# Optimization experiments

Hardware: AMD Instinct MI355X
Metric: run time of the kernel (lower is better)

Reference implementation:

```python
import jax, jax.numpy as jnp
import numpy as np

N = 100000      # nodes
E = 1600000     # edges (avg degree 16)
IN = 128        # in_channels
C = 32          # out_channels per head
H = 4           # heads
NEG_SLOPE = 0.2 # PyG GATConv leaky_relu slope


def setup_inputs() -> dict:
    key = jax.random.key(0)
    k = jax.random.split(key, 6)
    x = jax.random.normal(k[0], (N, IN), jnp.float32)
    edge_index = jax.random.randint(k[1], (2, E), 0, N, jnp.int32)
    # glorot-ish init for learned params
    W = jax.random.normal(k[2], (IN, H * C), jnp.float32) * (2.0 / (IN + H * C)) ** 0.5
    att_src = jax.random.normal(k[3], (H, C), jnp.float32) * (1.0 / C) ** 0.5
    att_dst = jax.random.normal(k[4], (H, C), jnp.float32) * (1.0 / C) ** 0.5
    bias = jnp.zeros((C,), jnp.float32)
    return {"x": x, "edge_index": edge_index, "W": W,
            "att_src": att_src, "att_dst": att_dst, "bias": bias}


def reference(x, edge_index, W, att_src, att_dst, bias):
    n = x.shape[0]
    h_heads, c = att_src.shape
    # add self loops (PyG GATConv default add_self_loops=True)
    loop = jnp.arange(n, dtype=edge_index.dtype)
    src = jnp.concatenate([edge_index[0], loop])
    dst = jnp.concatenate([edge_index[1], loop])
    # shared linear projection for src and dst (single-tensor input in PyG)
    h = (x @ W).reshape(n, h_heads, c)                 # [N,H,C]
    a_src = jnp.sum(h * att_src, axis=-1)              # [N,H]
    a_dst = jnp.sum(h * att_dst, axis=-1)              # [N,H]
    # per-edge attention logits
    e = jax.nn.leaky_relu(a_src[src] + a_dst[dst], NEG_SLOPE)  # [E',H]
    # segment softmax over incoming edges of each dst node
    m = jax.ops.segment_max(e, dst, num_segments=n)    # [N,H]
    m = jax.lax.stop_gradient(jnp.where(jnp.isfinite(m), m, 0.0))
    p = jnp.exp(e - m[dst])
    denom = jax.ops.segment_sum(p, dst, num_segments=n)
    alpha = p / (denom[dst] + 1e-16)                   # [E',H]
    # weighted message scatter-add
    msg = h[src] * alpha[:, :, None]                   # [E',H,C]
    out = jax.ops.segment_sum(msg, dst, num_segments=n)  # [N,H,C]
    out = out.mean(axis=1) + bias                      # concat=False -> head mean
    return jax.nn.relu(out)                            # trailing act layer
```

## Files before the change

### kernel.cpp

```cpp
#include <hip/hip_runtime.h>

#define NODES 100000
#define NEDGE 1600000
#define ET (NEDGE + NODES)
#define INC 128
#define CC 32
#define HH 4
#define NEG 0.2f
#define CAP 48
#define PB 512
#define BB 1024
#define BSTRIDE (BB * 256)
#define NPASS 7

typedef __attribute__((ext_vector_type(8))) short short8;
typedef __attribute__((ext_vector_type(4))) float f32x4;
typedef __attribute__((ext_vector_type(8))) unsigned short u16x8;

static __device__ inline unsigned short f2bf(float f) {
    unsigned u = __float_as_uint(f);
    u += 0x7FFFu + ((u >> 16) & 1u);
    return (unsigned short)(u >> 16);
}
static __device__ inline float bf2f(unsigned short s) {
    return __uint_as_float((unsigned)s << 16);
}
static __device__ inline float lexp(float v) {
    v = v > 0.f ? v : NEG * v;
    return __expf(v);
}

__global__ __launch_bounds__(256) void k_mega(const float* __restrict__ x,
        const float* __restrict__ W, const float* __restrict__ att_src,
        const float* __restrict__ att_dst, const int* __restrict__ ei,
        unsigned short* __restrict__ hb, float* __restrict__ av,
        int* __restrict__ deg, int* __restrict__ bucket) {
    const int tid = threadIdx.x;

    if (blockIdx.x >= PB) {
        const int bid = blockIdx.x - PB;
        const int e0 = bid * 256 + tid;
        int sv[NPASS], dv[NPASS], slot[NPASS];
        #pragma unroll
        for (int p = 0; p < NPASS; ++p) {
            int e = e0 + p * BSTRIDE;
            sv[p] = -1;
            if (e < ET) {
                if (e < NEDGE) { sv[p] = ei[e]; dv[p] = ei[NEDGE + e]; }
                else           { sv[p] = e - NEDGE; dv[p] = e - NEDGE; }
            }
        }
        #pragma unroll
        for (int p = 0; p < NPASS; ++p)
            if (sv[p] >= 0) slot[p] = atomicAdd(&deg[dv[p]], 1);
        #pragma unroll
        for (int p = 0; p < NPASS; ++p)
            if (sv[p] >= 0) bucket[dv[p] * CAP + slot[p]] = sv[p];
        return;
    }

    __shared__ unsigned short Wt[128][136];
    __shared__ unsigned short Axt[8][128];

    for (int i = tid; i < 128 * 128; i += 256) {
        int k = i >> 7, c = i & 127;
        Wt[c][k] = f2bf(W[i]);
    }
    for (int t = tid; t < 512; t += 256) {
        int k = t >> 2, hd = t & 3;
        float ss = 0.f, sd = 0.f;
        const float* wr = W + k * 128 + hd * 32;
        for (int c = 0; c < 32; ++c) {
            ss = fmaf(wr[c], att_src[hd * 32 + c], ss);
            sd = fmaf(wr[c], att_dst[hd * 32 + c], sd);
        }
        Axt[hd][k] = f2bf(ss);
        Axt[4 + hd][k] = f2bf(sd);
    }
    __syncthreads();

    const int w    = tid >> 6;
    const int lane = tid & 63;
    const int quad = lane >> 4;
    const int l15  = lane & 15;
    const int pid  = blockIdx.x;

    for (int base = pid * 64; base < NODES; base += PB * 64) {
        const int arow = base + w * 16 + l15;
        short8 af[4];
        if (arow < NODES) {
            const float* xp = x + (size_t)arow * INC + quad * 8;
            #pragma unroll
            for (int kt = 0; kt < 4; ++kt) {
                float4 u = *(const float4*)(xp + kt * 32);
                float4 v = *(const float4*)(xp + kt * 32 + 4);
                short8 a;
                a[0] = (short)f2bf(u.x); a[1] = (short)f2bf(u.y);
                a[2] = (short)f2bf(u.z); a[3] = (short)f2bf(u.w);
                a[4] = (short)f2bf(v.x); a[5] = (short)f2bf(v.y);
                a[6] = (short)f2bf(v.z); a[7] = (short)f2bf(v.w);
                af[kt] = a;
            }
        } else {
            #pragma unroll
            for (int kt = 0; kt < 4; ++kt) af[kt] = (short8){0,0,0,0,0,0,0,0};
        }

        f32x4 accs[8];
        #pragma unroll
        for (int ct = 0; ct < 8; ++ct) {
            const int gcol = ct * 16 + l15;
            f32x4 acc = {0.f, 0.f, 0.f, 0.f};
            #pragma unroll
            for (int kt = 0; kt < 4; ++kt) {
                short8 bf = *(short8*)(&Wt[gcol][kt * 32 + quad * 8]);
                acc = __builtin_amdgcn_mfma_f32_16x16x32_bf16(af[kt], bf, acc, 0, 0, 0);
            }
            accs[ct] = acc;
        }

        f32x4 acc9 = {0.f, 0.f, 0.f, 0.f};
        #pragma unroll
        for (int kt = 0; kt < 4; ++kt) {
            short8 bf = (short8){0,0,0,0,0,0,0,0};
            if (l15 < 8)
                bf = *(short8*)(&Axt[l15][kt * 32 + quad * 8]);
            acc9 = __builtin_amdgcn_mfma_f32_16x16x32_bf16(af[kt], bf, acc9, 0, 0, 0);
        }

        const int orow = base + w * 16 + quad * 4;

        #pragma unroll
        for (int reg = 0; reg < 4; ++reg) {
            int r = orow + reg;
            if (r < NODES) {
                if (l15 < 8) av[(size_t)r * 8 + l15] = acc9[reg];
                ushort4 lo, hi;
                lo.x = f2bf(accs[0][reg]); lo.y = f2bf(accs[2][reg]);
                lo.z = f2bf(accs[4][reg]); lo.w = f2bf(accs[6][reg]);
                hi.x = f2bf(accs[1][reg]); hi.y = f2bf(accs[3][reg]);
                hi.z = f2bf(accs[5][reg]); hi.w = f2bf(accs[7][reg]);
                *(ushort4*)(hb + (size_t)r * INC + l15 * 4) = lo;
                *(ushort4*)(hb + (size_t)r * INC + (16 + l15) * 4) = hi;
            }
        }
    }
}

__global__ __launch_bounds__(256) void k_scatter(const int* __restrict__ bucket,
        const int* __restrict__ deg, const unsigned short* __restrict__ hb,
        const float* __restrict__ av, const float* __restrict__ bias,
        float* __restrict__ out) {
    const int n = blockIdx.x * 16 + (threadIdx.x >> 4);
    const int l = threadIdx.x & 15;
    const int cbase = n * CAP;
    const int cnt = deg[n];
    const float4 ad = *(const float4*)(av + (size_t)n * 8 + 4);

    float acc[8] = {0.f,0.f,0.f,0.f,0.f,0.f,0.f,0.f};
    float den[4] = {0.f,0.f,0.f,0.f};

    int i = 0;
    for (; i + 2 <= cnt; i += 2) {
        int s0 = bucket[cbase + i];
        int s1 = bucket[cbase + i + 1];
        float4 as0 = *(const float4*)(av + (size_t)s0 * 8);
        float4 as1 = *(const float4*)(av + (size_t)s1 * 8);
        u16x8 h0 = *(const u16x8*)(hb + (size_t)s0 * INC + l * 8);
        u16x8 h1 = *(const u16x8*)(hb + (size_t)s1 * INC + l * 8);
        float p0 = lexp(as0.x + ad.x), p1 = lexp(as0.y + ad.y);
        float p2 = lexp(as0.z + ad.z), p3 = lexp(as0.w + ad.w);
        den[0] += p0; den[1] += p1; den[2] += p2; den[3] += p3;
        acc[0] = fmaf(p0, bf2f(h0[0]), acc[0]);
        acc[1] = fmaf(p1, bf2f(h0[1]), acc[1]);
        acc[2] = fmaf(p2, bf2f(h0[2]), acc[2]);
        acc[3] = fmaf(p3, bf2f(h0[3]), acc[3]);
        acc[4] = fmaf(p0, bf2f(h0[4]), acc[4]);
        acc[5] = fmaf(p1, bf2f(h0[5]), acc[5]);
        acc[6] = fmaf(p2, bf2f(h0[6]), acc[6]);
        acc[7] = fmaf(p3, bf2f(h0[7]), acc[7]);
        float q0 = lexp(as1.x + ad.x), q1 = lexp(as1.y + ad.y);
        float q2 = lexp(as1.z + ad.z), q3 = lexp(as1.w + ad.w);
        den[0] += q0; den[1] += q1; den[2] += q2; den[3] += q3;
        acc[0] = fmaf(q0, bf2f(h1[0]), acc[0]);
        acc[1] = fmaf(q1, bf2f(h1[1]), acc[1]);
        acc[2] = fmaf(q2, bf2f(h1[2]), acc[2]);
        acc[3] = fmaf(q3, bf2f(h1[3]), acc[3]);
        acc[4] = fmaf(q0, bf2f(h1[4]), acc[4]);
        acc[5] = fmaf(q1, bf2f(h1[5]), acc[5]);
        acc[6] = fmaf(q2, bf2f(h1[6]), acc[6]);
        acc[7] = fmaf(q3, bf2f(h1[7]), acc[7]);
    }
    if (i < cnt) {
        int s0 = bucket[cbase + i];
        float4 as0 = *(const float4*)(av + (size_t)s0 * 8);
        u16x8 h0 = *(const u16x8*)(hb + (size_t)s0 * INC + l * 8);
        float p0 = lexp(as0.x + ad.x), p1 = lexp(as0.y + ad.y);
        float p2 = lexp(as0.z + ad.z), p3 = lexp(as0.w + ad.w);
        den[0] += p0; den[1] += p1; den[2] += p2; den[3] += p3;
        acc[0] = fmaf(p0, bf2f(h0[0]), acc[0]);
        acc[1] = fmaf(p1, bf2f(h0[1]), acc[1]);
        acc[2] = fmaf(p2, bf2f(h0[2]), acc[2]);
        acc[3] = fmaf(p3, bf2f(h0[3]), acc[3]);
        acc[4] = fmaf(p0, bf2f(h0[4]), acc[4]);
        acc[5] = fmaf(p1, bf2f(h0[5]), acc[5]);
        acc[6] = fmaf(p2, bf2f(h0[6]), acc[6]);
        acc[7] = fmaf(p3, bf2f(h0[7]), acc[7]);
    }

    float r0 = 1.f / (den[0] + 1e-16f);
    float r1 = 1.f / (den[1] + 1e-16f);
    float r2 = 1.f / (den[2] + 1e-16f);
    float r3 = 1.f / (den[3] + 1e-16f);
    float o0 = 0.25f * (acc[0]*r0 + acc[1]*r1 + acc[2]*r2 + acc[3]*r3)
             + bias[2*l];
    float o1 = 0.25f * (acc[4]*r0 + acc[5]*r1 + acc[6]*r2 + acc[7]*r3)
             + bias[2*l + 1];
    float2 ov;
    ov.x = o0 > 0.f ? o0 : 0.f;
    ov.y = o1 > 0.f ? o1 : 0.f;
    *(float2*)(out + (size_t)n * CC + 2*l) = ov;
}

extern "C" void kernel_launch(void* const* d_in, const int* in_sizes, int n_in,
                              void* d_out, int out_size, void* d_ws, size_t ws_size,
                              hipStream_t stream) {
    const float* x       = (const float*)d_in[0];
    const int*   ei      = (const int*)d_in[1];
    const float* W       = (const float*)d_in[2];
    const float* att_src = (const float*)d_in[3];
    const float* att_dst = (const float*)d_in[4];
    const float* bias    = (const float*)d_in[5];
    float* out = (float*)d_out;

    int* bucket         = (int*)d_ws;
    unsigned short* hb  = (unsigned short*)(bucket + (size_t)NODES * CAP);
    float* av           = (float*)(hb + (size_t)NODES * INC);
    int* deg            = (int*)(av + (size_t)NODES * 8);

    hipMemsetAsync(deg, 0, sizeof(int) * (size_t)NODES, stream);

    k_mega<<<PB + BB, 256, 0, stream>>>(x, W, att_src, att_dst, ei, hb, av, deg, bucket);
    k_scatter<<<NODES / 16, 256, 0, stream>>>(bucket, deg, hb, av, bias, out);
}
```

Baseline: 297.4 us.

## Interleave projection and bucketing blocks in fused kernel with larger grid

The fused kernel now assigns block roles by blockIdx mod 8, five projection blocks to three edge-bucketing blocks, instead of a contiguous split. The grid grows to 2048 blocks, with more projection blocks and more passes per bucketing thread. The aim is to mix compute-heavy GEMM work with atomic-heavy edge binning on every CU and balance their tail. More projection blocks add redundant per-block LDS setup of the folded attention weights.

Result: faster. 270.3 us (-9.1%).

```diff
diff --git a/kernel.cpp b/kernel.cpp
--- a/kernel.cpp
+++ b/kernel.cpp
@@ -8,10 +8,13 @@
 #define HH 4
 #define NEG 0.2f
 #define CAP 48
-#define PB 512
-#define BB 1024
-#define BSTRIDE (BB * 256)
-#define NPASS 7
+#define GRID 2048
+#define NPX 5
+#define NP (GRID / 8 * NPX)
+#define NBK (GRID - NP)
+#define PSTRIDE (NP * 64)
+#define BSTRIDE (NBK * 256)
+#define NPASS 9
 
 typedef __attribute__((ext_vector_type(8))) short short8;
 typedef __attribute__((ext_vector_type(4))) float f32x4;
@@ -36,10 +39,11 @@
         unsigned short* __restrict__ hb, float* __restrict__ av,
         int* __restrict__ deg, int* __restrict__ bucket) {
     const int tid = threadIdx.x;
-
-    if (blockIdx.x >= PB) {
-        const int bid = blockIdx.x - PB;
-        const int e0 = bid * 256 + tid;
+    const int r8  = blockIdx.x & 7;
+
+    if (r8 >= NPX) {
+        const int qid = (blockIdx.x >> 3) * 3 + (r8 - NPX);
+        const int e0 = qid * 256 + tid;
         int sv[NPASS], dv[NPASS], slot[NPASS];
         #pragma unroll
         for (int p = 0; p < NPASS; ++p) {
@@ -83,9 +87,9 @@
     const int lane = tid & 63;
     const int quad = lane >> 4;
     const int l15  = lane & 15;
-    const int pid  = blockIdx.x;
-
-    for (int base = pid * 64; base < NODES; base += PB * 64) {
+    const int pid  = (blockIdx.x >> 3) * NPX + r8;
+
+    for (int base = pid * 64; base < NODES; base += PSTRIDE) {
         const int arow = base + w * 16 + l15;
         short8 af[4];
         if (arow < NODES) {
@@ -132,16 +136,16 @@
 
         #pragma unroll
         for (int reg = 0; reg < 4; ++reg) {
-            int r = orow + reg;
-            if (r < NODES) {
-                if (l15 < 8) av[(size_t)r * 8 + l15] = acc9[reg];
+            int rr = orow + reg;
+            if (rr < NODES) {
+                if (l15 < 8) av[(size_t)rr * 8 + l15] = acc9[reg];
                 ushort4 lo, hi;
                 lo.x = f2bf(accs[0][reg]); lo.y = f2bf(accs[2][reg]);
                 lo.z = f2bf(accs[4][reg]); lo.w = f2bf(accs[6][reg]);
                 hi.x = f2bf(accs[1][reg]); hi.y = f2bf(accs[3][reg]);
                 hi.z = f2bf(accs[5][reg]); hi.w = f2bf(accs[7][reg]);
-                *(ushort4*)(hb + (size_t)r * INC + l15 * 4) = lo;
-                *(ushort4*)(hb + (size_t)r * INC + (16 + l15) * 4) = hi;
+                *(ushort4*)(hb + (size_t)rr * INC + l15 * 4) = lo;
+                *(ushort4*)(hb + (size_t)rr * INC + (16 + l15) * 4) = hi;
             }
         }
     }
@@ -240,6 +244,6 @@
 
     hipMemsetAsync(deg, 0, sizeof(int) * (size_t)NODES, stream);
 
-    k_mega<<<PB + BB, 256, 0, stream>>>(x, W, att_src, att_dst, ei, hb, av, deg, bucket);
+    k_mega<<<GRID, 256, 0, stream>>>(x, W, att_src, att_dst, ei, hb, av, deg, bucket);
     k_scatter<<<NODES / 16, 256, 0, stream>>>(bucket, deg, hb, av, bias, out);
 }
```
